# Optimization experiments

Measured on AMD Instinct MI355X. Metric: run time of the kernel, lower is better.

Reference implementation:

```python
import jax, jax.numpy as jnp
import numpy as np

D_MODEL = 1024
NUM_HEADS = 16
D_K = D_MODEL // NUM_HEADS
B, S = 2, 2048
NEG = -1e9


def setup_inputs() -> dict:
    key = jax.random.key(0)
    ks = jax.random.split(key, 12)
    sc = 1.0 / np.sqrt(D_MODEL)
    inp = {
        'Q': jax.random.normal(ks[0], (B, S, D_MODEL), jnp.float32),
        'K': jax.random.normal(ks[1], (B, S, D_MODEL), jnp.float32),
        'V': jax.random.normal(ks[2], (B, S, D_MODEL), jnp.float32),
        # causal additive mask: 1.0 above diagonal -> scores += mask * -1e9
        'mask': jnp.triu(jnp.ones((S, S), jnp.float32), k=1),
        'Wq': jax.random.normal(ks[3], (D_MODEL, D_MODEL), jnp.float32) * sc,
        'bq': jnp.zeros((D_MODEL,), jnp.float32),
        'Wk': jax.random.normal(ks[4], (D_MODEL, D_MODEL), jnp.float32) * sc,
        'bk': jnp.zeros((D_MODEL,), jnp.float32),
        'Wv': jax.random.normal(ks[5], (D_MODEL, D_MODEL), jnp.float32) * sc,
        'bv': jnp.zeros((D_MODEL,), jnp.float32),
        'Wo': jax.random.normal(ks[6], (D_MODEL, D_MODEL), jnp.float32) * sc,
        'bo': jnp.zeros((D_MODEL,), jnp.float32),
    }
    return inp


def _split_heads(x):
    # [B,S,D] -> [B,H,S,d_k]
    b, s, _ = x.shape
    return x.reshape(b, s, NUM_HEADS, D_K).transpose(0, 2, 1, 3)


def reference(Q, K, V, mask, Wq, bq, Wk, bk, Wv, bv, Wo, bo):
    # torch Linear: y = x @ W.T + b
    q = _split_heads(Q @ Wq.T + bq)  # [B,H,S,d_k]
    k = _split_heads(K @ Wk.T + bk)
    v = _split_heads(V @ Wv.T + bv)
    scores = jnp.einsum('bhqd,bhkd->bhqk', q, k) / np.sqrt(D_K)
    scores = scores + mask * NEG  # mask broadcasts over [B,H]
    probs = jax.nn.softmax(scores, axis=-1)
    attn = jnp.einsum('bhqk,bhkd->bhqd', probs, v)  # [B,H,S,d_k]
    attn = attn.transpose(0, 2, 1, 3).reshape(Q.shape[0], Q.shape[1], D_MODEL)
    return attn @ Wo.T + bo
```

## Files before the change

kernel.cpp:

```cpp
#include <hip/hip_runtime.h>
#include <cstdint>
#include <cstddef>

#define D_MODEL 1024
#define NHEADS  16
#define DK      64
#define BATCH   2
#define SEQ     2048
#define MTOT    (BATCH*SEQ)
#define NT      (SEQ/64)

typedef unsigned short u16;
typedef __attribute__((ext_vector_type(8))) __bf16 bf16x8;
typedef __attribute__((ext_vector_type(4))) float  f32x4;
typedef __attribute__((ext_vector_type(4))) uint32_t u32x4;

#define QSCALE 0.18033688f

static __device__ __forceinline__ void gload16(const void* g, void* l) {
  __builtin_amdgcn_global_load_lds((const __attribute__((address_space(1))) void*)g,
                                   (__attribute__((address_space(3))) void*)l,
                                   16, 0, 0);
}

__global__ void cast_all_kernel(
    const float* __restrict__ Q, const float* __restrict__ K, const float* __restrict__ V,
    const float* __restrict__ Wq, const float* __restrict__ Wk,
    const float* __restrict__ Wv, const float* __restrict__ Wo,
    u16* __restrict__ dstX, u16* __restrict__ dstW) {
  constexpr int NX = MTOT * D_MODEL;
  constexpr int NW = D_MODEL * D_MODEL;
  const int i = (blockIdx.x * blockDim.x + threadIdx.x) * 4;
  const float* src;
  u16* dst;
  if (i < 3 * NX) {
    dst = dstX + i;
    src = (i < NX) ? Q + i : (i < 2 * NX) ? K + (i - NX) : V + (i - 2 * NX);
  } else {
    const int j = i - 3 * NX;
    dst = dstW + j;
    const int ws = j >> 20;
    const int jo = j & (NW - 1);
    src = (ws == 0) ? Wq + jo : (ws == 1) ? Wk + jo : (ws == 2) ? Wv + jo : Wo + jo;
  }
  float4 f = *reinterpret_cast<const float4*>(src);
  union { __bf16 h[4]; ushort4 s; } o;
  o.h[0] = (__bf16)f.x; o.h[1] = (__bf16)f.y; o.h[2] = (__bf16)f.z; o.h[3] = (__bf16)f.w;
  *reinterpret_cast<ushort4*>(dst) = o.s;
}

__global__ __launch_bounds__(256, 3) void gemm_qkv(
    const u16* __restrict__ A,
    const u16* __restrict__ W0, const u16* __restrict__ W1, const u16* __restrict__ W2,
    const float* __restrict__ b0, const float* __restrict__ b1, const float* __restrict__ b2,
    u16* __restrict__ out_q, u16* __restrict__ out_k, u16* __restrict__ out_v) {
  constexpr int K = 1024;
  constexpr int EP = 136;
  __shared__ __align__(16) u16 smem[128 * EP];
  u16* lA = smem;
  u16* lB = smem + 128 * 64;
  const int w = threadIdx.x >> 6, lane = threadIdx.x & 63;
  const int blockM = blockIdx.x * 128, blockN = blockIdx.y * 128;
  const int sel = blockIdx.x >> 5;
  const u16*  Bt   = sel == 0 ? W0 : (sel == 1 ? W1 : W2);
  const float* bias = sel == 0 ? b0 : (sel == 1 ? b1 : b2);
  const int wm = (w >> 1) * 64, wn = (w & 1) * 64;
  f32x4 acc[4][4] = {};
  for (int kt = 0; kt < K; kt += 64) {
#pragma unroll
    for (int it = 0; it < 4; ++it) {
      int rowb = w * 32 + it * 8;
      int row  = rowb + (lane >> 3);
      int cc   = (lane & 7) * 8;
      gload16(A  + (size_t)(blockM + row) * K + kt + cc, &lA[rowb * 64]);
      gload16(Bt + (size_t)(blockN + row) * K + kt + cc, &lB[rowb * 64]);
    }
    __syncthreads();
#pragma unroll
    for (int kc = 0; kc < 2; ++kc) {
      bf16x8 af[4], bfr[4];
#pragma unroll
      for (int i = 0; i < 4; ++i)
        af[i] = *(const bf16x8*)&lA[(wm + i * 16 + (lane & 15)) * 64 + kc * 32 + (lane >> 4) * 8];
#pragma unroll
      for (int j = 0; j < 4; ++j)
        bfr[j] = *(const bf16x8*)&lB[(wn + j * 16 + (lane & 15)) * 64 + kc * 32 + (lane >> 4) * 8];
#pragma unroll
      for (int i = 0; i < 4; ++i)
#pragma unroll
        for (int j = 0; j < 4; ++j)
          acc[i][j] = __builtin_amdgcn_mfma_f32_16x16x32_bf16(af[i], bfr[j], acc[i][j], 0, 0, 0);
    }
    __syncthreads();
  }
  if (sel == 2) {
#pragma unroll
    for (int i = 0; i < 4; ++i)
#pragma unroll
      for (int j = 0; j < 4; ++j) {
        int m0 = blockM + wm + i * 16 + (lane >> 4) * 4;
        int n  = blockN + wn + j * 16 + (lane & 15);
        int ml = m0 & (MTOT - 1);
        int b = ml >> 11, s = ml & (SEQ - 1), h = n >> 6, d = n & (DK - 1);
        union { __bf16 h4[4]; ushort4 s4; } st;
#pragma unroll
        for (int r = 0; r < 4; ++r) st.h4[r] = (__bf16)(acc[i][j][r] + bias[n]);
        *(ushort4*)&out_v[(((size_t)(b * NHEADS + h)) * DK + d) * SEQ + s] = st.s4;
      }
  } else {
#pragma unroll
    for (int i = 0; i < 4; ++i)
#pragma unroll
      for (int j = 0; j < 4; ++j) {
        int n = blockN + wn + j * 16 + (lane & 15);
        float bn = bias[n];
#pragma unroll
        for (int r = 0; r < 4; ++r) {
          float val = acc[i][j][r] + bn;
          if (sel == 0) val *= QSCALE;
          union { __bf16 h2; u16 u; } cv; cv.h2 = (__bf16)val;
          smem[(wm + i * 16 + (lane >> 4) * 4 + r) * EP + wn + j * 16 + (lane & 15)] = cv.u;
        }
      }
    __syncthreads();
    u16* outqk = sel ? out_k : out_q;
    const int t = threadIdx.x;
    const int seg = t & 15;
    const int h = (blockN >> 6) + (seg >> 3);
    const int d = (seg & 7) * 8;
#pragma unroll
    for (int pass = 0; pass < 8; ++pass) {
      const int row = pass * 16 + (t >> 4);
      u32x4 vdat = *(const u32x4*)&smem[row * EP + seg * 8];
      const int m = blockM + row;
      const int ml = m & (MTOT - 1);
      const int b = ml >> 11, s = ml & (SEQ - 1);
      *(u32x4*)&outqk[(((size_t)(b * NHEADS + h)) * SEQ + s) * DK + d] = vdat;
    }
  }
}

__global__ __launch_bounds__(256, 2) void gemm_out(
    const u16* __restrict__ A, const u16* __restrict__ Bt,
    const float* __restrict__ bias, float* __restrict__ outp) {
  constexpr int K = 1024, N = 1024;
  __shared__ __align__(16) u16 lA[64 * 64];
  __shared__ __align__(16) u16 lB[128 * 64];
  const int w = threadIdx.x >> 6, lane = threadIdx.x & 63;
  const int blockM = blockIdx.x * 64, blockN = blockIdx.y * 128;
  const int wm = (w >> 1) * 32, wn = (w & 1) * 64;
  f32x4 acc[2][4] = {};
  for (int kt = 0; kt < K; kt += 64) {
#pragma unroll
    for (int it = 0; it < 2; ++it) {
      int rowb = w * 16 + it * 8;
      int row  = rowb + (lane >> 3);
      int cc   = (lane & 7) * 8;
      gload16(A + (size_t)(blockM + row) * K + kt + cc, &lA[rowb * 64]);
    }
#pragma unroll
    for (int it = 0; it < 4; ++it) {
      int rowb = w * 32 + it * 8;
      int row  = rowb + (lane >> 3);
      int cc   = (lane & 7) * 8;
      gload16(Bt + (size_t)(blockN + row) * K + kt + cc, &lB[rowb * 64]);
    }
    __syncthreads();
#pragma unroll
    for (int kc = 0; kc < 2; ++kc) {
      bf16x8 af[2], bfr[4];
#pragma unroll
      for (int i = 0; i < 2; ++i)
        af[i] = *(const bf16x8*)&lA[(wm + i * 16 + (lane & 15)) * 64 + kc * 32 + (lane >> 4) * 8];
#pragma unroll
      for (int j = 0; j < 4; ++j)
        bfr[j] = *(const bf16x8*)&lB[(wn + j * 16 + (lane & 15)) * 64 + kc * 32 + (lane >> 4) * 8];
#pragma unroll
      for (int i = 0; i < 2; ++i)
#pragma unroll
        for (int j = 0; j < 4; ++j)
          acc[i][j] = __builtin_amdgcn_mfma_f32_16x16x32_bf16(af[i], bfr[j], acc[i][j], 0, 0, 0);
    }
    __syncthreads();
  }
#pragma unroll
  for (int i = 0; i < 2; ++i)
#pragma unroll
    for (int j = 0; j < 4; ++j)
#pragma unroll
      for (int r = 0; r < 4; ++r) {
        int m = blockM + wm + i * 16 + (lane >> 4) * 4 + r;
        int n = blockN + wn + j * 16 + (lane & 15);
        outp[(size_t)m * N + n] = acc[i][j][r] + bias[n];
      }
}

static __device__ __forceinline__ void stage_kv(
    const u16* kp, const u16* vp, int j0,
    u16* bufK, u16* bufV, int w, int lane) {
  const int rsub = lane >> 3;
  const int cl = ((lane & 7) ^ rsub) << 3;
#pragma unroll
  for (int it = 0; it < 2; ++it) {
    const int rowb = w * 16 + it * 8;
    gload16(kp + (size_t)(j0 + rowb + rsub) * DK + cl, bufK + rowb * 64);
    gload16(vp + (size_t)(rowb + rsub) * SEQ + j0 + cl, bufV + rowb * 64);
  }
}

__global__ __launch_bounds__(256, 5) void attn_kernel(
    const u16* __restrict__ qh, const u16* __restrict__ kh,
    const u16* __restrict__ vt, u16* __restrict__ attnb,
    float* __restrict__ pO, float* __restrict__ pML) {
  __shared__ __align__(16) u16 lKV[2][2][64 * 64];
  const int w = threadIdx.x >> 6, lane = threadIdx.x & 63;
  const int g = lane >> 4, q15 = lane & 15;
  const int lid = blockIdx.x;
  const int xcd = lid & 7;
  const int idx = lid >> 3;
  const int p   = idx & 3;
  const int slot = idx >> 2;
  const int bh = xcd * 4 + p;
  int qt, t_begin, t_end, half, split;
  if (slot < 32) {
    qt = 16 + (slot >> 1); half = slot & 1; split = 1;
    const int ntt = qt + 1, h0 = ntt >> 1;
    t_begin = half ? h0 : 0;
    t_end   = half ? ntt : h0;
  } else {
    qt = 47 - slot; half = 0; split = 0;
    t_begin = 0; t_end = qt + 1;
  }
  const int b = bh >> 4, h = bh & 15;
  const u16* qp = qh + (size_t)bh * SEQ * DK;
  const u16* kp = kh + (size_t)bh * SEQ * DK;
  const u16* vp = vt + (size_t)bh * DK * SEQ;

  const int qbase = qt * 64;
  const int qrow = qbase + w * 16 + q15;
  bf16x8 aq[2];
  const u16* qr = qp + (size_t)qrow * DK;
#pragma unroll
  for (int kc = 0; kc < 2; ++kc)
    aq[kc] = *(const bf16x8*)(qr + kc * 32 + g * 8);

  float m_run = -1e30f, l_run = 0.f;
  f32x4 oacc[4] = {};
  stage_kv(kp, vp, t_begin * 64, lKV[t_begin & 1][0], lKV[t_begin & 1][1], w, lane);

  for (int t = t_begin; t < t_end; ++t) {
    __syncthreads();
    const int cur = t & 1;
    if (t + 1 < t_end)
      stage_kv(kp, vp, (t + 1) * 64, lKV[cur ^ 1][0], lKV[cur ^ 1][1], w, lane);
    const u16* bK = lKV[cur][0];
    const u16* bV = lKV[cur][1];

    f32x4 sacc[4] = {};
    __builtin_amdgcn_s_setprio(1);
#pragma unroll
    for (int kc = 0; kc < 2; ++kc)
#pragma unroll
      for (int nb = 0; nb < 4; ++nb) {
        const int rr = nb * 16 + q15;
        const int cc = kc * 4 + g;
        bf16x8 kf = *(const bf16x8*)&bK[rr * 64 + ((cc ^ (rr & 7)) << 3)];
        sacc[nb] = __builtin_amdgcn_mfma_f32_16x16x32_bf16(kf, aq[kc], sacc[nb], 0, 0, 0);
      }
    __builtin_amdgcn_s_setprio(0);

    float pvv[4][4];
    float mx = -1e30f;
    if (t == qt) {
#pragma unroll
      for (int nb = 0; nb < 4; ++nb)
#pragma unroll
        for (int r = 0; r < 4; ++r) {
          float s = sacc[nb][r];
          if (t * 64 + nb * 16 + g * 4 + r > qrow) s = -1e30f;
          pvv[nb][r] = s;
          mx = fmaxf(mx, s);
        }
    } else {
#pragma unroll
      for (int nb = 0; nb < 4; ++nb)
#pragma unroll
        for (int r = 0; r < 4; ++r) {
          float s = sacc[nb][r];
          pvv[nb][r] = s;
          mx = fmaxf(mx, s);
        }
    }
    mx = fmaxf(mx, __shfl_xor(mx, 16));
    mx = fmaxf(mx, __shfl_xor(mx, 32));
    if (__any(mx > m_run + 8.0f)) {
      const float mn = fmaxf(m_run, mx);
      const float alpha = __builtin_amdgcn_exp2f(m_run - mn);
      m_run = mn;
      l_run *= alpha;
#pragma unroll
      for (int nd = 0; nd < 4; ++nd)
#pragma unroll
        for (int r = 0; r < 4; ++r) oacc[nd][r] *= alpha;
    }
    float rs = 0.f;
#pragma unroll
    for (int nb = 0; nb < 4; ++nb)
#pragma unroll
      for (int r = 0; r < 4; ++r) {
        float e = __builtin_amdgcn_exp2f(pvv[nb][r] - m_run);
        pvv[nb][r] = e;
        rs += e;
      }
    rs += __shfl_xor(rs, 16);
    rs += __shfl_xor(rs, 32);
    l_run += rs;

    uint32_t pk[4][2];
#pragma unroll
    for (int nb = 0; nb < 4; ++nb) {
      union { __bf16 h2[2]; uint32_t u; } t0, t1;
      t0.h2[0] = (__bf16)pvv[nb][0]; t0.h2[1] = (__bf16)pvv[nb][1];
      t1.h2[0] = (__bf16)pvv[nb][2]; t1.h2[1] = (__bf16)pvv[nb][3];
      pk[nb][0] = t0.u; pk[nb][1] = t1.u;
    }

#pragma unroll
    for (int jc = 0; jc < 2; ++jc) {
      union { u32x4 u; bf16x8 bvec; } pf;
      const int sgbase = (g & 1) * 2;
#pragma unroll
      for (int W = 0; W < 4; ++W) {
        const int src = (sgbase + (W >> 1)) * 16 + q15;
        const uint32_t lo = (uint32_t)__shfl((int)pk[2 * jc][W & 1], src, 64);
        const uint32_t hi = (uint32_t)__shfl((int)pk[2 * jc + 1][W & 1], src, 64);
        pf.u[W] = (lane >= 32) ? hi : lo;
      }
      __builtin_amdgcn_s_setprio(1);
#pragma unroll
      for (int nd = 0; nd < 4; ++nd) {
        const int rr = nd * 16 + q15;
        const int cc = jc * 4 + g;
        bf16x8 vf = *(const bf16x8*)&bV[rr * 64 + ((cc ^ (rr & 7)) << 3)];
        oacc[nd] = __builtin_amdgcn_mfma_f32_16x16x32_bf16(vf, pf.bvec, oacc[nd], 0, 0, 0);
      }
      __builtin_amdgcn_s_setprio(0);
    }
  }

  if (!split) {
    const float rl = 1.0f / l_run;
#pragma unroll
    for (int nd = 0; nd < 4; ++nd) {
      union { __bf16 h4[4]; ushort4 s4; } st;
      st.h4[0] = (__bf16)(oacc[nd][0] * rl);
      st.h4[1] = (__bf16)(oacc[nd][1] * rl);
      st.h4[2] = (__bf16)(oacc[nd][2] * rl);
      st.h4[3] = (__bf16)(oacc[nd][3] * rl);
      *(ushort4*)&attnb[((size_t)(b * SEQ + qrow)) * D_MODEL + h * 64 + nd * 16 + g * 4] = st.s4;
    }
  } else {
    const int pid = ((bh << 4) + (qt - 16)) * 2 + half;
    float* po = pO + (size_t)pid * 4096 + (w * 16 + q15) * 64;
#pragma unroll
    for (int nd = 0; nd < 4; ++nd)
      *(f32x4*)(po + nd * 16 + g * 4) = oacc[nd];
    if (g == 0) {
      float2 ml; ml.x = m_run; ml.y = l_run;
      ((float2*)pML)[pid * 64 + w * 16 + q15] = ml;
    }
  }
}

__global__ __launch_bounds__(256) void attn_combine(
    const float* __restrict__ pO, const float* __restrict__ pML,
    u16* __restrict__ attnb) {
  const int blk = blockIdx.x;
  const int bh = blk >> 4, qti = blk & 15;
  const int qt = 16 + qti;
  const int b = bh >> 4, h = bh & 15;
  const int pid0 = ((bh << 4) + qti) * 2;
  const int t = threadIdx.x;
  const int row = t >> 2, c0 = (t & 3) * 16;
  const float2 ml0 = ((const float2*)pML)[pid0 * 64 + row];
  const float2 ml1 = ((const float2*)pML)[(pid0 + 1) * 64 + row];
  const float M = fmaxf(ml0.x, ml1.x);
  const float w0 = __builtin_amdgcn_exp2f(ml0.x - M);
  const float w1 = __builtin_amdgcn_exp2f(ml1.x - M);
  const float inv = 1.0f / (ml0.y * w0 + ml1.y * w1);
  const float s0 = w0 * inv, s1 = w1 * inv;
  const float* O0 = pO + (size_t)pid0 * 4096 + row * 64 + c0;
  const float* O1 = O0 + 4096;
  u16* dst = attnb + ((size_t)(b * SEQ + qt * 64 + row)) * D_MODEL + h * 64 + c0;
#pragma unroll
  for (int c = 0; c < 4; ++c) {
    float4 a  = *(const float4*)(O0 + c * 4);
    float4 d2 = *(const float4*)(O1 + c * 4);
    union { __bf16 h4[4]; ushort4 s4; } st;
    st.h4[0] = (__bf16)(a.x * s0 + d2.x * s1);
    st.h4[1] = (__bf16)(a.y * s0 + d2.y * s1);
    st.h4[2] = (__bf16)(a.z * s0 + d2.z * s1);
    st.h4[3] = (__bf16)(a.w * s0 + d2.w * s1);
    *(ushort4*)(dst + c * 4) = st.s4;
  }
}

extern "C" void kernel_launch(void* const* d_in, const int* in_sizes, int n_in,
                              void* d_out, int out_size, void* d_ws, size_t ws_size,
                              hipStream_t stream) {
  (void)in_sizes; (void)n_in; (void)out_size; (void)ws_size;
  const float* Q  = (const float*)d_in[0];
  const float* K  = (const float*)d_in[1];
  const float* V  = (const float*)d_in[2];
  const float* Wq = (const float*)d_in[4];
  const float* bq = (const float*)d_in[5];
  const float* Wk = (const float*)d_in[6];
  const float* bk = (const float*)d_in[7];
  const float* Wv = (const float*)d_in[8];
  const float* bv = (const float*)d_in[9];
  const float* Wo = (const float*)d_in[10];
  const float* bo = (const float*)d_in[11];

  char* ws = (char*)d_ws;
  size_t off = 0;
  auto carve = [&](size_t bytes) { char* p = ws + off; off += bytes; return p; };
  const size_t szX = (size_t)MTOT * D_MODEL * 2;
  const size_t szW = (size_t)D_MODEL * D_MODEL * 2;
  u16* Qb  = (u16*)carve(szX);
  u16* Kb  = (u16*)carve(szX);
  u16* Vb  = (u16*)carve(szX);
  u16* Wqb = (u16*)carve(szW);
  u16* Wkb = (u16*)carve(szW);
  u16* Wvb = (u16*)carve(szW);
  u16* Wob = (u16*)carve(szW);
  u16* qhB = (u16*)carve(szX);
  u16* khB = (u16*)carve(szX);
  u16* vtB = (u16*)carve(szX);
  u16* attnb = Qb;
  float* pO  = (float*)Kb;
  float* pML = (float*)Wqb;
  (void)Wkb; (void)Wvb;

  const int nTot = 3 * MTOT * D_MODEL + 4 * D_MODEL * D_MODEL;
  cast_all_kernel<<<nTot / 1024, 256, 0, stream>>>(Q, K, V, Wq, Wk, Wv, Wo, Qb, Wqb);

  gemm_qkv<<<dim3(3 * MTOT / 128, D_MODEL / 128), 256, 0, stream>>>(
      Qb, Wqb, Wkb, Wvb, bq, bk, bv, qhB, khB, vtB);

  attn_kernel<<<1536, 256, 0, stream>>>(qhB, khB, vtB, attnb, pO, pML);

  attn_combine<<<512, 256, 0, stream>>>(pO, pML, attnb);

  gemm_out<<<dim3(MTOT / 64, D_MODEL / 128), 256, 0, stream>>>(attnb, Wob, bo, (float*)d_out);
}
```

Baseline: 122.9 us.

## Split attention KV range into fixed 8-tile chunks with bf16 partials

Replaces the two-way split of the upper query tiles with a uniform chunking: every work item covers at most 8 KV tiles, so query tiles 8 and above are split into 2-4 chunks. This gives 2560 balanced blocks, scheduled longest first, instead of 1536 uneven ones. Partial outputs are now stored as bf16 rather than fp32 to cut the partial write and read traffic, and the combine kernel merges up to four partials per row. The cost is more combine work, extra partial traffic for mid-length tiles, and some precision loss in the partials.

After: 125.1 us. About the same (+1.8%).

```diff
diff --git a/kernel.cpp b/kernel.cpp
--- a/kernel.cpp
+++ b/kernel.cpp
@@ -21,6 +21,10 @@
   __builtin_amdgcn_global_load_lds((const __attribute__((address_space(1))) void*)g,
                                    (__attribute__((address_space(3))) void*)l,
                                    16, 0, 0);
+}
+
+static __device__ __forceinline__ float bfu(u16 x) {
+  union { uint32_t u; float f; } v; v.u = (uint32_t)x << 16; return v.f;
 }
 
 __global__ void cast_all_kernel(
@@ -211,7 +215,7 @@
 __global__ __launch_bounds__(256, 5) void attn_kernel(
     const u16* __restrict__ qh, const u16* __restrict__ kh,
     const u16* __restrict__ vt, u16* __restrict__ attnb,
-    float* __restrict__ pO, float* __restrict__ pML) {
+    u16* __restrict__ pO, float2* __restrict__ pML) {
   __shared__ __align__(16) u16 lKV[2][2][64 * 64];
   const int w = threadIdx.x >> 6, lane = threadIdx.x & 63;
   const int g = lane >> 4, q15 = lane & 15;
@@ -219,18 +223,17 @@
   const int xcd = lid & 7;
   const int idx = lid >> 3;
   const int p   = idx & 3;
-  const int slot = idx >> 2;
+  const int sraw = idx >> 2;
+  const int s = 79 - sraw;
   const int bh = xcd * 4 + p;
-  int qt, t_begin, t_end, half, split;
-  if (slot < 32) {
-    qt = 16 + (slot >> 1); half = slot & 1; split = 1;
-    const int ntt = qt + 1, h0 = ntt >> 1;
-    t_begin = half ? h0 : 0;
-    t_end   = half ? ntt : h0;
-  } else {
-    qt = 47 - slot; half = 0; split = 0;
-    t_begin = 0; t_end = qt + 1;
-  }
+  int qt, c, nch;
+  if (s < 8)       { qt = s;                c = 0;           nch = 1; }
+  else if (s < 24) { qt = 8 + ((s - 8) >> 1); c = (s - 8) & 1; nch = 2; }
+  else if (s < 48) { int u = s - 24; int q3 = u / 3; qt = 16 + q3; c = u - q3 * 3; nch = 3; }
+  else             { int u = s - 48; qt = 24 + (u >> 2); c = u & 3; nch = 4; }
+  const int t_begin = c * 8;
+  const int t_end   = min(t_begin + 8, qt + 1);
+  const int split   = nch > 1;
   const int b = bh >> 4, h = bh & 15;
   const u16* qp = qh + (size_t)bh * SEQ * DK;
   const u16* kp = kh + (size_t)bh * SEQ * DK;
@@ -276,19 +279,19 @@
       for (int nb = 0; nb < 4; ++nb)
 #pragma unroll
         for (int r = 0; r < 4; ++r) {
-          float s = sacc[nb][r];
-          if (t * 64 + nb * 16 + g * 4 + r > qrow) s = -1e30f;
-          pvv[nb][r] = s;
-          mx = fmaxf(mx, s);
+          float ss = sacc[nb][r];
+          if (t * 64 + nb * 16 + g * 4 + r > qrow) ss = -1e30f;
+          pvv[nb][r] = ss;
+          mx = fmaxf(mx, ss);
         }
     } else {
 #pragma unroll
       for (int nb = 0; nb < 4; ++nb)
 #pragma unroll
         for (int r = 0; r < 4; ++r) {
-          float s = sacc[nb][r];
-          pvv[nb][r] = s;
-          mx = fmaxf(mx, s);
+          float ss = sacc[nb][r];
+          pvv[nb][r] = ss;
+          mx = fmaxf(mx, ss);
         }
     }
     mx = fmaxf(mx, __shfl_xor(mx, 16));
@@ -360,49 +363,78 @@
       *(ushort4*)&attnb[((size_t)(b * SEQ + qrow)) * D_MODEL + h * 64 + nd * 16 + g * 4] = st.s4;
     }
   } else {
-    const int pid = ((bh << 4) + (qt - 16)) * 2 + half;
-    float* po = pO + (size_t)pid * 4096 + (w * 16 + q15) * 64;
-#pragma unroll
-    for (int nd = 0; nd < 4; ++nd)
-      *(f32x4*)(po + nd * 16 + g * 4) = oacc[nd];
+    const int pid = bh * 72 + (s - 8);
+    u16* po = pO + (size_t)pid * 4096 + (w * 16 + q15) * 64;
+#pragma unroll
+    for (int nd = 0; nd < 4; ++nd) {
+      union { __bf16 h4[4]; ushort4 s4; } st;
+      st.h4[0] = (__bf16)oacc[nd][0];
+      st.h4[1] = (__bf16)oacc[nd][1];
+      st.h4[2] = (__bf16)oacc[nd][2];
+      st.h4[3] = (__bf16)oacc[nd][3];
+      *(ushort4*)(po + nd * 16 + g * 4) = st.s4;
+    }
     if (g == 0) {
       float2 ml; ml.x = m_run; ml.y = l_run;
-      ((float2*)pML)[pid * 64 + w * 16 + q15] = ml;
+      pML[(size_t)pid * 64 + w * 16 + q15] = ml;
     }
   }
 }
 
 __global__ __launch_bounds__(256) void attn_combine(
-    const float* __restrict__ pO, const float* __restrict__ pML,
+    const u16* __restrict__ pO, const float2* __restrict__ pML,
     u16* __restrict__ attnb) {
   const int blk = blockIdx.x;
-  const int bh = blk >> 4, qti = blk & 15;
-  const int qt = 16 + qti;
+  const int bh = blk / 24, qti = blk - (blk / 24) * 24;
+  const int qt = 8 + qti;
   const int b = bh >> 4, h = bh & 15;
-  const int pid0 = ((bh << 4) + qti) * 2;
+  int nch, sbase;
+  if (qt < 16)      { nch = 2; sbase = 8 + (qt - 8) * 2; }
+  else if (qt < 24) { nch = 3; sbase = 24 + (qt - 16) * 3; }
+  else              { nch = 4; sbase = 48 + (qt - 24) * 4; }
+  const int pbase = bh * 72 + (sbase - 8);
   const int t = threadIdx.x;
   const int row = t >> 2, c0 = (t & 3) * 16;
-  const float2 ml0 = ((const float2*)pML)[pid0 * 64 + row];
-  const float2 ml1 = ((const float2*)pML)[(pid0 + 1) * 64 + row];
-  const float M = fmaxf(ml0.x, ml1.x);
-  const float w0 = __builtin_amdgcn_exp2f(ml0.x - M);
-  const float w1 = __builtin_amdgcn_exp2f(ml1.x - M);
-  const float inv = 1.0f / (ml0.y * w0 + ml1.y * w1);
-  const float s0 = w0 * inv, s1 = w1 * inv;
-  const float* O0 = pO + (size_t)pid0 * 4096 + row * 64 + c0;
-  const float* O1 = O0 + 4096;
+
+  float m[4] = {-1e30f, -1e30f, -1e30f, -1e30f};
+  float l[4] = {0.f, 0.f, 0.f, 0.f};
+  float M = -1e30f;
+#pragma unroll
+  for (int i = 0; i < 4; ++i)
+    if (i < nch) {
+      float2 ml = pML[(size_t)(pbase + i) * 64 + row];
+      m[i] = ml.x; l[i] = ml.y;
+      M = fmaxf(M, ml.x);
+    }
+  float denom = 0.f, sc[4];
+#pragma unroll
+  for (int i = 0; i < 4; ++i) {
+    sc[i] = __builtin_amdgcn_exp2f(m[i] - M);
+    denom += l[i] * sc[i];
+  }
+  const float inv = 1.0f / denom;
+  float out[16] = {};
+#pragma unroll
+  for (int i = 0; i < 4; ++i)
+    if (i < nch) {
+      const float scale = sc[i] * inv;
+      const u16* pp = pO + (size_t)(pbase + i) * 4096 + row * 64 + c0;
+      u32x4 d0 = *(const u32x4*)pp;
+      u32x4 d1 = *(const u32x4*)(pp + 8);
+#pragma unroll
+      for (int k = 0; k < 4; ++k) {
+        out[2 * k + 0] += scale * bfu((u16)(d0[k] & 0xffffu));
+        out[2 * k + 1] += scale * bfu((u16)(d0[k] >> 16));
+        out[8 + 2 * k + 0] += scale * bfu((u16)(d1[k] & 0xffffu));
+        out[8 + 2 * k + 1] += scale * bfu((u16)(d1[k] >> 16));
+      }
+    }
+  union { __bf16 h8[8]; u32x4 s; } o0, o1;
+#pragma unroll
+  for (int k = 0; k < 8; ++k) { o0.h8[k] = (__bf16)out[k]; o1.h8[k] = (__bf16)out[8 + k]; }
   u16* dst = attnb + ((size_t)(b * SEQ + qt * 64 + row)) * D_MODEL + h * 64 + c0;
-#pragma unroll
-  for (int c = 0; c < 4; ++c) {
-    float4 a  = *(const float4*)(O0 + c * 4);
-    float4 d2 = *(const float4*)(O1 + c * 4);
-    union { __bf16 h4[4]; ushort4 s4; } st;
-    st.h4[0] = (__bf16)(a.x * s0 + d2.x * s1);
-    st.h4[1] = (__bf16)(a.y * s0 + d2.y * s1);
-    st.h4[2] = (__bf16)(a.z * s0 + d2.z * s1);
-    st.h4[3] = (__bf16)(a.w * s0 + d2.w * s1);
-    *(ushort4*)(dst + c * 4) = st.s4;
-  }
+  *(u32x4*)dst = o0.s;
+  *(u32x4*)(dst + 8) = o1.s;
 }
 
 extern "C" void kernel_launch(void* const* d_in, const int* in_sizes, int n_in,
@@ -437,8 +469,8 @@
   u16* khB = (u16*)carve(szX);
   u16* vtB = (u16*)carve(szX);
   u16* attnb = Qb;
-  float* pO  = (float*)Kb;
-  float* pML = (float*)Wqb;
+  u16*    pO  = (u16*)Kb;
+  float2* pML = (float2*)((char*)Kb + (size_t)19 * 1024 * 1024);
   (void)Wkb; (void)Wvb;
 
   const int nTot = 3 * MTOT * D_MODEL + 4 * D_MODEL * D_MODEL;
@@ -447,9 +479,9 @@
   gemm_qkv<<<dim3(3 * MTOT / 128, D_MODEL / 128), 256, 0, stream>>>(
       Qb, Wqb, Wkb, Wvb, bq, bk, bv, qhB, khB, vtB);
 
-  attn_kernel<<<1536, 256, 0, stream>>>(qhB, khB, vtB, attnb, pO, pML);
-
-  attn_combine<<<512, 256, 0, stream>>>(pO, pML, attnb);
+  attn_kernel<<<2560, 256, 0, stream>>>(qhB, khB, vtB, attnb, pO, pML);
+
+  attn_combine<<<768, 256, 0, stream>>>(pO, pML, attnb);
 
   gemm_out<<<dim3(MTOT / 64, D_MODEL / 128), 256, 0, stream>>>(attnb, Wob, bo, (float*)d_out);
 }
```
